# Kernel tuning notes

Measured on AMD Instinct MI355X. Metric: run time of the kernel, lower is better.

Reference implementation:

```python
import jax, jax.numpy as jnp
import numpy as np

N = 100000       # nodes
DEG = 16         # fixed out/in degree used to build CSR
E = N * DEG      # edges
D_IN = 128       # in_feats
D_OUT = 256      # out_feats
K = 32           # maxk k_value


def _xavier_uniform(key, shape, gain):
    fan_out, fan_in = shape
    bound = gain * np.sqrt(6.0 / (fan_in + fan_out))
    return jax.random.uniform(key, shape, jnp.float32, -bound, bound)


def setup_inputs() -> dict:
    key = jax.random.key(0)
    ks = jax.random.split(key, 6)
    feat = jax.random.normal(ks[0], (N, D_IN), jnp.float32)
    topk_values = jax.random.uniform(ks[1], (N, K), jnp.float32)
    topk_indices = jax.random.randint(ks[2], (N, K), 0, D_IN).astype(jnp.int32)
    # CSR graph: fixed degree -> indptr is arange*DEG; random destinations
    indptr = (jnp.arange(N + 1) * DEG).astype(jnp.int32)
    indices = jax.random.randint(ks[3], (E,), 0, N).astype(jnp.int32)
    # set_graph_data: csr weight[e] = 1 / clamp(in_degree(dst), 1)
    in_deg = jax.ops.segment_sum(jnp.ones(E, jnp.float32), indices, num_segments=N)
    in_deg = jnp.maximum(in_deg, 1.0)
    csr_values = 1.0 / in_deg[indices]
    gain = np.sqrt(2.0)  # calculate_gain('relu')
    w_neigh = _xavier_uniform(ks[4], (D_OUT, D_IN), gain)
    w_self = _xavier_uniform(ks[5], (D_OUT, D_IN), gain)
    b_self = jnp.zeros((D_OUT,), jnp.float32)
    return {"feat": feat, "topk_values": topk_values, "csr_values": csr_values,
            "w_neigh": w_neigh, "w_self": w_self, "b_self": b_self,
            "topk_indices": topk_indices, "indptr": indptr, "indices": indices}


def reference(feat, topk_values, csr_values, w_neigh, w_self, b_self,
              topk_indices, indptr, indices):
    # Densify the k-sparse MaxK features: x[n, topk_indices[n, j]] = topk_values[n, j]
    x = jnp.zeros((N, D_IN), feat.dtype).at[
        jnp.arange(N)[:, None], topk_indices].add(topk_values)
    # Edge-weight-normalized SpMM over CSR: out[row] += w[e] * x[col[e]]
    row_ids = jnp.repeat(jnp.arange(N), jnp.diff(indptr), total_repeat_length=E)
    msgs = x[indices] * csr_values[:, None]          # [E, D_IN]
    agg = jax.ops.segment_sum(msgs, row_ids, num_segments=N)  # [N, D_IN]
    # lin_before_mp is False (in_feats <= out_feats): project after aggregation
    h_neigh = agg @ w_neigh.T                        # [N, D_OUT]
    rst = feat @ w_self.T + b_self + h_neigh         # fc_self(h_self) + h_neigh
    return rst
```

## Files before the change

kernel.cpp:

```cpp
#include <hip/hip_runtime.h>
#include <hip/hip_bf16.h>
#include <stdint.h>

#define N_NODES 100000
#define DEG 16
#define D_IN 128
#define D_OUT 256
#define K_TOP 32
#define K_CAT 256

typedef __attribute__((ext_vector_type(8))) short short8;
typedef __attribute__((ext_vector_type(4))) float floatx4;

__device__ __forceinline__ unsigned pack_bf16_rne(float f) {
    union { float f; unsigned u; } c; c.f = f;
    unsigned u = c.u;
    return (u + 0x7fffu + ((u >> 16) & 1u)) >> 16;
}
__device__ __forceinline__ float bf16lo_to_f(unsigned lo16) {
    union { unsigned u; float f; } c; c.u = lo16 << 16; return c.f;
}

__global__ __launch_bounds__(256) void k_packw(const float* __restrict__ w_self,
                                               const float* __restrict__ w_neigh,
                                               unsigned short* __restrict__ bmat) {
    int o = blockIdx.x;
    int k = threadIdx.x;
    float v = (k < D_IN) ? w_self[o * D_IN + k] : w_neigh[o * D_IN + (k - D_IN)];
    bmat[o * K_CAT + k] = (unsigned short)pack_bf16_rne(v);
}

__global__ __launch_bounds__(128) void k_densify(const float* __restrict__ topk_v,
                                                 const int* __restrict__ topk_i,
                                                 unsigned short* __restrict__ xbf) {
    __shared__ float sx[128 * 128];
    int t = threadIdx.x;
    int row = blockIdx.x * 128 + t;
    for (int i = t; i < 128 * 128; i += 128) sx[i] = 0.f;
    __syncthreads();
    if (row < N_NODES) {
        const float* v = topk_v + (size_t)row * K_TOP;
        const int*  ix = topk_i + (size_t)row * K_TOP;
        float* myrow = sx + t * 128;
        #pragma unroll
        for (int j = 0; j < K_TOP; ++j) myrow[ix[j]] += v[j];
    }
    __syncthreads();
    size_t base = (size_t)blockIdx.x * (128 * 128);
    for (int i = t; i < 128 * 128; i += 128) {
        int r = blockIdx.x * 128 + (i >> 7);
        if (r < N_NODES) xbf[base + i] = (unsigned short)pack_bf16_rne(sx[i]);
    }
}

__global__ __launch_bounds__(256) void k_spmm(const float* __restrict__ feat,
                                              const float* __restrict__ csr_w,
                                              const int* __restrict__ col_idx,
                                              const unsigned short* __restrict__ xbf,
                                              unsigned short* __restrict__ abf) {
    int wave = threadIdx.x >> 6;
    int lane = threadIdx.x & 63;
    int row  = blockIdx.x * 4 + wave;
    if (row >= N_NODES) return;

    const float2 f2 = *(const float2*)(feat + (size_t)row * D_IN + 2 * lane);
    unsigned fp = pack_bf16_rne(f2.x) | (pack_bf16_rne(f2.y) << 16);
    ((unsigned*)(abf + (size_t)row * K_CAT))[lane] = fp;

    int c = 0; float w = 0.f;
    if (lane < DEG) {
        c = col_idx[row * DEG + lane];
        w = csr_w[row * DEG + lane];
    }
    float a0 = 0.f, a1 = 0.f;
    #pragma unroll
    for (int e = 0; e < DEG; ++e) {
        int col  = __shfl(c, e);
        float we = __shfl(w, e);
        unsigned v = ((const unsigned*)(xbf + (size_t)col * D_IN))[lane];
        a0 += we * bf16lo_to_f(v & 0xffffu);
        a1 += we * bf16lo_to_f(v >> 16);
    }
    unsigned ap = pack_bf16_rne(a0) | (pack_bf16_rne(a1) << 16);
    ((unsigned*)(abf + (size_t)row * K_CAT + D_IN))[lane] = ap;
}

#define BM 128
#define BN 128
#define BK 32
#define LDP 40

__global__ __launch_bounds__(256) void k_gemm(const unsigned short* __restrict__ abf,
                                              const unsigned short* __restrict__ bmat,
                                              const float* __restrict__ bias,
                                              float* __restrict__ out) {
    __shared__ unsigned short As[BM * LDP];
    __shared__ unsigned short Bs[BN * LDP];
    int t = threadIdx.x;
    int lane = t & 63, wave = t >> 6;
    int wr = wave >> 1, wc = wave & 1;
    int row0 = blockIdx.x * BM;
    int col0 = blockIdx.y * BN;

    floatx4 acc[4][4];
    #pragma unroll
    for (int i = 0; i < 4; ++i)
        #pragma unroll
        for (int j = 0; j < 4; ++j)
            acc[i][j] = (floatx4){0.f, 0.f, 0.f, 0.f};

    int quad = lane >> 4;
    int l16  = lane & 15;

    for (int kt = 0; kt < K_CAT; kt += BK) {
        __syncthreads();
        #pragma unroll
        for (int p = 0; p < 2; ++p) {
            int chunk = t + p * 256;
            int r  = chunk >> 2;
            int ko = (chunk & 3) * 8;
            uint4 av = make_uint4(0u, 0u, 0u, 0u);
            int gr = row0 + r;
            if (gr < N_NODES)
                av = *(const uint4*)(abf + (size_t)gr * K_CAT + kt + ko);
            *(uint4*)&As[r * LDP + ko] = av;
            uint4 bv = *(const uint4*)(bmat + (size_t)(col0 + r) * K_CAT + kt + ko);
            *(uint4*)&Bs[r * LDP + ko] = bv;
        }
        __syncthreads();

        short8 afr[4], bfr[4];
        #pragma unroll
        for (int i = 0; i < 4; ++i) {
            int m = wr * 64 + i * 16 + l16;
            afr[i] = *(const short8*)&As[m * LDP + quad * 8];
        }
        #pragma unroll
        for (int j = 0; j < 4; ++j) {
            int n = wc * 64 + j * 16 + l16;
            bfr[j] = *(const short8*)&Bs[n * LDP + quad * 8];
        }
        #pragma unroll
        for (int i = 0; i < 4; ++i)
            #pragma unroll
            for (int j = 0; j < 4; ++j)
                acc[i][j] = __builtin_amdgcn_mfma_f32_16x16x32_bf16(afr[i], bfr[j], acc[i][j], 0, 0, 0);
    }

    #pragma unroll
    for (int j = 0; j < 4; ++j) {
        int cg = col0 + wc * 64 + j * 16 + l16;
        float bv = bias[cg];
        #pragma unroll
        for (int i = 0; i < 4; ++i) {
            int mbase = row0 + wr * 64 + i * 16 + quad * 4;
            #pragma unroll
            for (int r = 0; r < 4; ++r) {
                int gr = mbase + r;
                if (gr < N_NODES) out[(size_t)gr * D_OUT + cg] = acc[i][j][r] + bv;
            }
        }
    }
}

extern "C" void kernel_launch(void* const* d_in, const int* in_sizes, int n_in,
                              void* d_out, int out_size, void* d_ws, size_t ws_size,
                              hipStream_t stream) {
    const float* feat    = (const float*)d_in[0];
    const float* topk_v  = (const float*)d_in[1];
    const float* csr_w   = (const float*)d_in[2];
    const float* w_neigh = (const float*)d_in[3];
    const float* w_self  = (const float*)d_in[4];
    const float* b_self  = (const float*)d_in[5];
    const int*   topk_i  = (const int*)d_in[6];
    const int*   indices = (const int*)d_in[8];
    float* out = (float*)d_out;

    unsigned short* xbf  = (unsigned short*)d_ws;
    unsigned short* abf  = xbf + (size_t)N_NODES * D_IN;
    unsigned short* bmat = abf + (size_t)N_NODES * K_CAT;

    k_packw<<<dim3(256), dim3(256), 0, stream>>>(w_self, w_neigh, bmat);
    k_densify<<<dim3((N_NODES + 127) / 128), dim3(128), 0, stream>>>(topk_v, topk_i, xbf);
    k_spmm<<<dim3(N_NODES / 4), dim3(256), 0, stream>>>(feat, csr_w, indices, xbf, abf);
    dim3 g((N_NODES + BM - 1) / BM, D_OUT / BN);
    k_gemm<<<g, dim3(256), 0, stream>>>(abf, bmat, b_self, out);
}
```

Before: 317.8 us.

## Rework densify as wave-per-row shuffle, batch SpMM gathers, widen GEMM tile to full N

Densify now assigns one wave per row and builds the dense row by shuffling the top-k entries and comparing indices, replacing the 64KB LDS scratch per block that limited occupancy. The feat-to-bf16 conversion moves from the SpMM kernel into densify. SpMM issues all 16 neighbour gathers before accumulating, which gives more memory-level parallelism. The GEMM tile grows to cover all 256 output columns, so each A tile is loaded once, at the cost of more accumulator registers (launch bounds set to 2 blocks per SM).

```diff
diff --git a/kernel.cpp b/kernel.cpp
--- a/kernel.cpp
+++ b/kernel.cpp
@@ -30,31 +30,39 @@
     bmat[o * K_CAT + k] = (unsigned short)pack_bf16_rne(v);
 }
 
-__global__ __launch_bounds__(128) void k_densify(const float* __restrict__ topk_v,
+__global__ __launch_bounds__(256) void k_densify(const float* __restrict__ topk_v,
                                                  const int* __restrict__ topk_i,
-                                                 unsigned short* __restrict__ xbf) {
-    __shared__ float sx[128 * 128];
-    int t = threadIdx.x;
-    int row = blockIdx.x * 128 + t;
-    for (int i = t; i < 128 * 128; i += 128) sx[i] = 0.f;
-    __syncthreads();
-    if (row < N_NODES) {
-        const float* v = topk_v + (size_t)row * K_TOP;
-        const int*  ix = topk_i + (size_t)row * K_TOP;
-        float* myrow = sx + t * 128;
-        #pragma unroll
-        for (int j = 0; j < K_TOP; ++j) myrow[ix[j]] += v[j];
-    }
-    __syncthreads();
-    size_t base = (size_t)blockIdx.x * (128 * 128);
-    for (int i = t; i < 128 * 128; i += 128) {
-        int r = blockIdx.x * 128 + (i >> 7);
-        if (r < N_NODES) xbf[base + i] = (unsigned short)pack_bf16_rne(sx[i]);
-    }
-}
-
-__global__ __launch_bounds__(256) void k_spmm(const float* __restrict__ feat,
-                                              const float* __restrict__ csr_w,
+                                                 const float* __restrict__ feat,
+                                                 unsigned short* __restrict__ xbf,
+                                                 unsigned short* __restrict__ abf) {
+    int wave = threadIdx.x >> 6;
+    int lane = threadIdx.x & 63;
+    int row  = blockIdx.x * 4 + wave;
+    if (row >= N_NODES) return;
+
+    int   ix = 0; float v = 0.f;
+    if (lane < K_TOP) {
+        ix = topk_i[row * K_TOP + lane];
+        v  = topk_v[row * K_TOP + lane];
+    }
+    const int c0 = 2 * lane, c1 = 2 * lane + 1;
+    float a0 = 0.f, a1 = 0.f;
+    #pragma unroll
+    for (int j = 0; j < K_TOP; ++j) {
+        int   idx = __shfl(ix, j);
+        float val = __shfl(v, j);
+        a0 += (idx == c0) ? val : 0.f;
+        a1 += (idx == c1) ? val : 0.f;
+    }
+    unsigned xp = pack_bf16_rne(a0) | (pack_bf16_rne(a1) << 16);
+    ((unsigned*)(xbf + (size_t)row * D_IN))[lane] = xp;
+
+    const float2 f2 = *(const float2*)(feat + (size_t)row * D_IN + c0);
+    unsigned fp = pack_bf16_rne(f2.x) | (pack_bf16_rne(f2.y) << 16);
+    ((unsigned*)(abf + (size_t)row * K_CAT))[lane] = fp;
+}
+
+__global__ __launch_bounds__(256) void k_spmm(const float* __restrict__ csr_w,
                                               const int* __restrict__ col_idx,
                                               const unsigned short* __restrict__ xbf,
                                               unsigned short* __restrict__ abf) {
@@ -63,50 +71,49 @@
     int row  = blockIdx.x * 4 + wave;
     if (row >= N_NODES) return;
 
-    const float2 f2 = *(const float2*)(feat + (size_t)row * D_IN + 2 * lane);
-    unsigned fp = pack_bf16_rne(f2.x) | (pack_bf16_rne(f2.y) << 16);
-    ((unsigned*)(abf + (size_t)row * K_CAT))[lane] = fp;
-
     int c = 0; float w = 0.f;
     if (lane < DEG) {
         c = col_idx[row * DEG + lane];
         w = csr_w[row * DEG + lane];
     }
+    unsigned vv[DEG];
+    #pragma unroll
+    for (int e = 0; e < DEG; ++e) {
+        int col = __shfl(c, e);
+        vv[e] = ((const unsigned*)(xbf + (size_t)col * D_IN))[lane];
+    }
     float a0 = 0.f, a1 = 0.f;
     #pragma unroll
     for (int e = 0; e < DEG; ++e) {
-        int col  = __shfl(c, e);
         float we = __shfl(w, e);
-        unsigned v = ((const unsigned*)(xbf + (size_t)col * D_IN))[lane];
-        a0 += we * bf16lo_to_f(v & 0xffffu);
-        a1 += we * bf16lo_to_f(v >> 16);
+        a0 += we * bf16lo_to_f(vv[e] & 0xffffu);
+        a1 += we * bf16lo_to_f(vv[e] >> 16);
     }
     unsigned ap = pack_bf16_rne(a0) | (pack_bf16_rne(a1) << 16);
     ((unsigned*)(abf + (size_t)row * K_CAT + D_IN))[lane] = ap;
 }
 
 #define BM 128
-#define BN 128
+#define BN 256
 #define BK 32
 #define LDP 40
 
-__global__ __launch_bounds__(256) void k_gemm(const unsigned short* __restrict__ abf,
-                                              const unsigned short* __restrict__ bmat,
-                                              const float* __restrict__ bias,
-                                              float* __restrict__ out) {
+__global__ __launch_bounds__(256, 2) void k_gemm(const unsigned short* __restrict__ abf,
+                                                 const unsigned short* __restrict__ bmat,
+                                                 const float* __restrict__ bias,
+                                                 float* __restrict__ out) {
     __shared__ unsigned short As[BM * LDP];
     __shared__ unsigned short Bs[BN * LDP];
     int t = threadIdx.x;
     int lane = t & 63, wave = t >> 6;
     int wr = wave >> 1, wc = wave & 1;
     int row0 = blockIdx.x * BM;
-    int col0 = blockIdx.y * BN;
-
-    floatx4 acc[4][4];
+
+    floatx4 acc[4][8];
     #pragma unroll
     for (int i = 0; i < 4; ++i)
         #pragma unroll
-        for (int j = 0; j < 4; ++j)
+        for (int j = 0; j < 8; ++j)
             acc[i][j] = (floatx4){0.f, 0.f, 0.f, 0.f};
 
     int quad = lane >> 4;
@@ -124,32 +131,38 @@
             if (gr < N_NODES)
                 av = *(const uint4*)(abf + (size_t)gr * K_CAT + kt + ko);
             *(uint4*)&As[r * LDP + ko] = av;
-            uint4 bv = *(const uint4*)(bmat + (size_t)(col0 + r) * K_CAT + kt + ko);
+        }
+        #pragma unroll
+        for (int p = 0; p < 4; ++p) {
+            int chunk = t + p * 256;
+            int r  = chunk >> 2;
+            int ko = (chunk & 3) * 8;
+            uint4 bv = *(const uint4*)(bmat + (size_t)r * K_CAT + kt + ko);
             *(uint4*)&Bs[r * LDP + ko] = bv;
         }
         __syncthreads();
 
-        short8 afr[4], bfr[4];
+        short8 afr[4], bfr[8];
         #pragma unroll
         for (int i = 0; i < 4; ++i) {
             int m = wr * 64 + i * 16 + l16;
             afr[i] = *(const short8*)&As[m * LDP + quad * 8];
         }
         #pragma unroll
-        for (int j = 0; j < 4; ++j) {
-            int n = wc * 64 + j * 16 + l16;
+        for (int j = 0; j < 8; ++j) {
+            int n = wc * 128 + j * 16 + l16;
             bfr[j] = *(const short8*)&Bs[n * LDP + quad * 8];
         }
         #pragma unroll
         for (int i = 0; i < 4; ++i)
             #pragma unroll
-            for (int j = 0; j < 4; ++j)
+            for (int j = 0; j < 8; ++j)
                 acc[i][j] = __builtin_amdgcn_mfma_f32_16x16x32_bf16(afr[i], bfr[j], acc[i][j], 0, 0, 0);
     }
 
     #pragma unroll
-    for (int j = 0; j < 4; ++j) {
-        int cg = col0 + wc * 64 + j * 16 + l16;
+    for (int j = 0; j < 8; ++j) {
+        int cg = wc * 128 + j * 16 + l16;
         float bv = bias[cg];
         #pragma unroll
         for (int i = 0; i < 4; ++i) {
@@ -181,8 +194,7 @@
     unsigned short* bmat = abf + (size_t)N_NODES * K_CAT;
 
     k_packw<<<dim3(256), dim3(256), 0, stream>>>(w_self, w_neigh, bmat);
-    k_densify<<<dim3((N_NODES + 127) / 128), dim3(128), 0, stream>>>(topk_v, topk_i, xbf);
-    k_spmm<<<dim3(N_NODES / 4), dim3(256), 0, stream>>>(feat, csr_w, indices, xbf, abf);
-    dim3 g((N_NODES + BM - 1) / BM, D_OUT / BN);
-    k_gemm<<<g, dim3(256), 0, stream>>>(abf, bmat, b_self, out);
-}
+    k_densify<<<dim3(N_NODES / 4), dim3(256), 0, stream>>>(topk_v, topk_i, feat, xbf, abf);
+    k_spmm<<<dim3(N_NODES / 4), dim3(256), 0, stream>>>(csr_w, indices, xbf, abf);
+    k_gemm<<<dim3((N_NODES + BM - 1) / BM), dim3(256), 0, stream>>>(abf, bmat, b_self, out);
+}
```

Result: slower. 325.2 us (+2.3%).
